# Kernel tuning notes

Hardware: AMD Instinct MI355X
Metric: run time of the kernel (lower is better)

The kernel has to match this reference:

```python
import jax, jax.numpy as jnp
import numpy as np

B, L, C, H = 1, 2048, 2048, 16
D = C // H
EPS = 1e-6
W0 = 30.0  # SIREN frequency

def rmsnorm(x, w, eps=EPS):
    return x * jax.lax.rsqrt(jnp.mean(x * x, axis=-1, keepdims=True) + eps) * w

def depth_rope(x, depth, base=10000.0):
    # same rotation for all positions, angle set by scalar layer depth
    d = x.shape[-1]
    half = d // 2
    freqs = 1.0 / base ** (jnp.arange(half, dtype=x.dtype) / half)
    ang = depth * freqs
    cos, sin = jnp.cos(ang), jnp.sin(ang)
    x1, x2 = x[..., :half], x[..., half:2 * half]
    return jnp.concatenate([x1 * cos - x2 * sin, x1 * sin + x2 * cos], axis=-1)

def setup_inputs() -> dict:
    key = jax.random.key(0)
    ks = jax.random.split(key, 13)
    s = 1.0 / np.sqrt(C)
    inp = {
        'x':  jax.random.normal(ks[0], (B, L, C), jnp.float32),
        'h0': jax.random.normal(ks[1], (B, L, C), jnp.float32),
        'h1': jax.random.normal(ks[2], (B, L, C), jnp.float32),
        'h2': jax.random.normal(ks[3], (B, L, C), jnp.float32),
        'Wq': jax.random.normal(ks[4], (C, C), jnp.float32) * s,
        'Wk': jax.random.normal(ks[5], (C, C), jnp.float32) * s,
        'Wv': jax.random.normal(ks[6], (C, C), jnp.float32) * s,
        'Wo': jax.random.normal(ks[7], (C, C), jnp.float32) * s,
        'qn_w': jnp.ones((D,), jnp.float32),
        'kn_w': jnp.ones((D,), jnp.float32),
        'on_w': jnp.ones((C,), jnp.float32),
        'sw1': jax.random.normal(ks[8], (1, C), jnp.float32),
        'sb1': jax.random.normal(ks[9], (C,), jnp.float32) * 0.01,
        'sw2': jax.random.normal(ks[10], (C, C), jnp.float32) * s,
        'sb2': jnp.zeros((C,), jnp.float32),
    }
    return inp

def reference(x, h0, h1, h2, Wq, Wk, Wv, Wo, qn_w, kn_w, on_w, sw1, sb1, sw2, sb2):
    history = [h0, h1, h2]
    q_src = history[-1]                      # [B,L,C]
    q_depth = len(history) - 1
    # Q path: proj -> per-head RMSNorm -> depth RoPE
    q = jnp.einsum('blc,oc->blo', q_src, Wq).reshape(B, L, H, D)
    q = depth_rope(rmsnorm(q, qn_w), q_depth)
    # K/V path over prior history entries (each with its own depth)
    k_parts, v_parts = [], []
    for depth_idx, kv in enumerate(history[:-1]):
        k_i = jnp.einsum('blc,oc->blo', kv, Wk).reshape(B, L, H, D)
        v_i = jnp.einsum('blc,oc->blo', kv, Wv).reshape(B, L, H, D)
        k_parts.append(depth_rope(rmsnorm(k_i, kn_w), depth_idx))
        v_parts.append(v_i)
    k = jnp.concatenate(k_parts, axis=1)     # [B,Lkv,H,D]
    v = jnp.concatenate(v_parts, axis=1)
    # full SDPA, default scale D^-0.5
    scores = jnp.einsum('bqhd,bkhd->bhqk', q, k) * (D ** -0.5)
    attn = jax.nn.softmax(scores, axis=-1)
    out = jnp.einsum('bhqk,bkhd->bqhd', attn, v).reshape(B, L, C)
    out = jnp.einsum('blc,oc->blo', out, Wo)
    # SIREN upsample to (L,): target length == L -> identity interpolation
    # plus sine-activated coordinate MLP (implicit positional field)
    coords = jnp.linspace(-1.0, 1.0, L, dtype=x.dtype)[:, None]   # [L,1]
    pos = jnp.sin(W0 * (coords @ sw1 + sb1)) @ sw2 + sb2           # [L,C]
    out = out + pos[None]
    return x + rmsnorm(out, on_w)
```

## Files before the change

### kernel.cpp

```cpp
#include <hip/hip_runtime.h>
#include <hip/hip_fp16.h>

#define LQ 2048
#define CDIM 2048
#define NHEAD 16
#define HDIM 128
#define LKEY 4096

typedef _Float16 f16x8 __attribute__((ext_vector_type(8)));
typedef float f32x4 __attribute__((ext_vector_type(4)));

#define GLOAD_LDS16(g, s) __builtin_amdgcn_global_load_lds( \
    (const __attribute__((address_space(1))) void*)(g),     \
    (__attribute__((address_space(3))) void*)(s), 16, 0, 0)

#define MFMA16(a, b, c) __builtin_amdgcn_mfma_f32_16x16x32_f16(a, b, c, 0, 0, 0)

__device__ __forceinline__ void storeC(float* p, float v) { *p = v; }
__device__ __forceinline__ void storeC(__half* p, float v) { *p = __float2half(v); }
__device__ __forceinline__ float toF(float v) { return v; }
__device__ __forceinline__ float toF(__half v) { return __half2float(v); }

template <typename OutT>
__global__ __launch_bounds__(256, 2) void gemm_bt(
    const __half* __restrict__ A, const __half* __restrict__ B,
    OutT* __restrict__ C, int lda, int ldb, int ldc, int K)
{
    __shared__ __align__(16) __half lA[128 * 64];
    __shared__ __align__(16) __half lB[128 * 64];
    const int tid  = threadIdx.x;
    const int lane = tid & 63;
    const int wave = tid >> 6;
    const int bm = blockIdx.x, bn = blockIdx.y;
    const int r = tid >> 3;
    const int g = tid & 7;
    const __half* gA = A + (long)(bm * 128 + r) * lda + ((g ^ (r & 7)) << 3);
    const __half* gB = B + (long)(bn * 128 + r) * ldb + ((g ^ (r & 7)) << 3);
    __half* lAp = lA + tid * 8;
    __half* lBp = lB + tid * 8;
    const int wr = (wave & 1) << 6;
    const int wc = (wave >> 1) << 6;
    const int l15 = lane & 15, quad = lane >> 4;

    f32x4 acc[4][4] = {};

    for (int kt = 0; kt < K; kt += 64) {
#pragma unroll
        for (int i = 0; i < 4; ++i) {
            GLOAD_LDS16(gA + (long)i * 32 * lda, lAp + i * 2048);
            GLOAD_LDS16(gB + (long)i * 32 * ldb, lBp + i * 2048);
        }
        gA += 64; gB += 64;
        __syncthreads();
#pragma unroll
        for (int kk = 0; kk < 2; ++kk) {
            f16x8 af[4], bfr[4];
#pragma unroll
            for (int mi = 0; mi < 4; ++mi) {
                const int m = wr + mi * 16 + l15;
                const int kg = kk * 4 + quad;
                af[mi] = *(const f16x8*)&lA[m * 64 + ((kg ^ (m & 7)) << 3)];
            }
#pragma unroll
            for (int ni = 0; ni < 4; ++ni) {
                const int n = wc + ni * 16 + l15;
                const int kg = kk * 4 + quad;
                bfr[ni] = *(const f16x8*)&lB[n * 64 + ((kg ^ (n & 7)) << 3)];
            }
#pragma unroll
            for (int mi = 0; mi < 4; ++mi)
#pragma unroll
                for (int ni = 0; ni < 4; ++ni)
                    acc[mi][ni] = MFMA16(af[mi], bfr[ni], acc[mi][ni]);
        }
        __syncthreads();
    }
    const int row0 = bm * 128 + wr + quad * 4;
    const int col0 = bn * 128 + wc + l15;
#pragma unroll
    for (int mi = 0; mi < 4; ++mi)
#pragma unroll
        for (int ni = 0; ni < 4; ++ni)
#pragma unroll
            for (int rx = 0; rx < 4; ++rx)
                storeC(&C[(long)(row0 + mi * 16 + rx) * ldc + col0 + ni * 16],
                       acc[mi][ni][rx]);
}

__global__ __launch_bounds__(256, 2) void attn_tile(
    const __half* __restrict__ Qf,
    const __half* __restrict__ Kf,
    const __half* __restrict__ Vt,
    float* __restrict__ Opart,
    float* __restrict__ lsum)
{
    __shared__ __align__(16) __half lK[64 * 128];
    __shared__ __align__(16) __half lV[128 * 64];
    __shared__ __align__(16) __half pL[4 * 2 * 16 * 72];

    const int tid  = threadIdx.x;
    const int lane = tid & 63;
    const int wave = tid >> 6;
    const int l15  = lane & 15;
    const int quad = lane >> 4;
    const int h  = blockIdx.y >> 1;
    const int kc = blockIdx.y & 1;
    const int q0 = blockIdx.x * 128 + wave * 32;

    f16x8 aq[2][4];
#pragma unroll
    for (int mt = 0; mt < 2; ++mt)
#pragma unroll
        for (int ks = 0; ks < 4; ++ks)
            aq[mt][ks] = *(const f16x8*)&Qf[(long)(q0 + mt * 16 + l15) * CDIM +
                                            h * HDIM + ks * 32 + quad * 8];

    const int rK = tid >> 4;
    const int gK = tid & 15;
    const __half* srcK = Kf + (long)(kc * 2048 + rK) * 4096 + h * HDIM +
                         ((gK ^ (rK & 15)) << 3);
    const int rV = tid >> 3;
    const int gV = tid & 7;
    const __half* srcV = Vt + (long)(h * HDIM + rV) * (long)LKEY + kc * 2048 +
                         ((gV ^ (rV & 7)) << 3);
    __half* dstK = lK + tid * 8;
    __half* dstV = lV + tid * 8;

    f32x4 accO[2][8] = {};
    f32x4 l_acc[2] = {};

    for (int st = 0; st < 32; ++st) {
#pragma unroll
        for (int i = 0; i < 4; ++i) {
            GLOAD_LDS16(srcK + (long)(st * 64 + i * 16) * 4096, dstK + i * 2048);
            GLOAD_LDS16(srcV + (long)i * 32 * LKEY + st * 64, dstV + i * 2048);
        }
        __syncthreads();
        f32x4 s[2][4];
#pragma unroll
        for (int mt = 0; mt < 2; ++mt)
#pragma unroll
            for (int nt = 0; nt < 4; ++nt)
                s[mt][nt] = (f32x4){-10.f, -10.f, -10.f, -10.f};
#pragma unroll
        for (int nt = 0; nt < 4; ++nt) {
            const int n = nt * 16 + l15;
#pragma unroll
            for (int ks = 0; ks < 4; ++ks) {
                const f16x8 kf = *(const f16x8*)
                    &lK[n * 128 + (((ks * 4 + quad) ^ (n & 15)) << 3)];
                s[0][nt] = MFMA16(aq[0][ks], kf, s[0][nt]);
                s[1][nt] = MFMA16(aq[1][ks], kf, s[1][nt]);
            }
        }
#pragma unroll
        for (int mt = 0; mt < 2; ++mt)
#pragma unroll
            for (int nt = 0; nt < 4; ++nt)
#pragma unroll
                for (int r2 = 0; r2 < 4; ++r2) {
                    const float p = __builtin_amdgcn_exp2f(s[mt][nt][r2]);
                    l_acc[mt][r2] += p;
                    pL[((wave * 2 + mt) * 16 + quad * 4 + r2) * 72 +
                       nt * 16 + l15] = __float2half(p);
                }
        f16x8 ap[2][2];
#pragma unroll
        for (int mt = 0; mt < 2; ++mt) {
            ap[mt][0] = *(const f16x8*)&pL[((wave * 2 + mt) * 16 + l15) * 72 + quad * 8];
            ap[mt][1] = *(const f16x8*)&pL[((wave * 2 + mt) * 16 + l15) * 72 + 32 + quad * 8];
        }
#pragma unroll
        for (int nt2 = 0; nt2 < 8; ++nt2) {
            const int n2 = nt2 * 16 + l15;
            const f16x8 v0 = *(const f16x8*)&lV[n2 * 64 + ((quad ^ (n2 & 7)) << 3)];
            const f16x8 v1 = *(const f16x8*)&lV[n2 * 64 + (((4 + quad) ^ (n2 & 7)) << 3)];
            accO[0][nt2] = MFMA16(ap[0][0], v0, accO[0][nt2]);
            accO[0][nt2] = MFMA16(ap[0][1], v1, accO[0][nt2]);
            accO[1][nt2] = MFMA16(ap[1][0], v0, accO[1][nt2]);
            accO[1][nt2] = MFMA16(ap[1][1], v1, accO[1][nt2]);
        }
        __syncthreads();
    }

#pragma unroll
    for (int mt = 0; mt < 2; ++mt)
#pragma unroll
        for (int r2 = 0; r2 < 4; ++r2) {
            float v = l_acc[mt][r2];
            v += __shfl_xor(v, 1);
            v += __shfl_xor(v, 2);
            v += __shfl_xor(v, 4);
            v += __shfl_xor(v, 8);
            if (l15 == 0)
                atomicAdd(&lsum[h * LQ + q0 + mt * 16 + quad * 4 + r2], v);
        }
    float* Cp = Opart + (long)kc * LQ * CDIM + h * HDIM;
#pragma unroll
    for (int mt = 0; mt < 2; ++mt)
#pragma unroll
        for (int nt2 = 0; nt2 < 8; ++nt2)
#pragma unroll
            for (int rx = 0; rx < 4; ++rx)
                Cp[(long)(q0 + mt * 16 + quad * 4 + rx) * CDIM + nt2 * 16 + l15] =
                    accO[mt][nt2][rx];
}

__global__ __launch_bounds__(256) void merge_o(
    const float* __restrict__ Op, const float* __restrict__ lsum,
    __half* __restrict__ a2)
{
    const int row = blockIdx.x;
    const int c0  = threadIdx.x * 8;
    const float inv = 1.0f / lsum[(c0 >> 7) * LQ + row];
    const float* p0 = Op + (long)row * CDIM + c0;
    const float* p1 = p0 + (long)LQ * CDIM;
    union { f16x8 v; _Float16 e[8]; } o;
#pragma unroll
    for (int j = 0; j < 8; ++j)
        o.e[j] = (_Float16)((p0[j] + p1[j]) * inv);
    *(f16x8*)&a2[(long)row * 4096 + c0] = o.v;
}

__global__ __launch_bounds__(256) void norm_rope(
    __half* __restrict__ X, const float* __restrict__ w,
    int stride, int nrows, int kmode, float oscale)
{
    const int gid  = blockIdx.x * 4 + (threadIdx.x >> 6);
    const int lane = threadIdx.x & 63;
    const int row  = gid >> 4;
    const int h    = gid & 15;
    if (row >= nrows) return;
    __half* p = X + (long)row * stride + h * HDIM;
    float x1 = __half2float(p[lane]);
    float x2 = __half2float(p[lane + 64]);
    float ss = x1 * x1 + x2 * x2;
#pragma unroll
    for (int off = 1; off < 64; off <<= 1) ss += __shfl_xor(ss, off);
    const float rn = rsqrtf(ss * (1.0f / 128.0f) + 1e-6f);
    x1 *= rn * w[lane];
    x2 *= rn * w[lane + 64];
    const int depth = kmode ? (row < LQ ? 0 : 1) : 2;
    const float freq = exp2f(-(float)lane * 0.20762050593045702f);
    const float ang = (float)depth * freq;
    float sn, cs;
    __sincosf(ang, &sn, &cs);
    p[lane]      = __float2half((x1 * cs - x2 * sn) * oscale);
    p[lane + 64] = __float2half((x1 * sn + x2 * cs) * oscale);
}

__global__ void cast_h4(const float* __restrict__ in, __half* __restrict__ out, int n) {
    const int i = (blockIdx.x * 256 + threadIdx.x) << 2;
    if (i >= n) return;
    const float4 v = *(const float4*)&in[i];
    out[i]     = __float2half(v.x);
    out[i + 1] = __float2half(v.y);
    out[i + 2] = __float2half(v.z);
    out[i + 3] = __float2half(v.w);
}

__global__ void cast_wo(const float* __restrict__ in, __half* __restrict__ out) {
    const int idx = blockIdx.x * 256 + threadIdx.x;
    const int o = idx >> 11, c = idx & 2047;
    out[((long)o << 12) + c] = __float2half(in[idx]);
}

template <typename InT>
__global__ __launch_bounds__(256) void transpose_h(
    const InT* __restrict__ in, long inStride, long inOff,
    __half* __restrict__ out, long outStride, long outOff)
{
    __shared__ float t[64][65];
    const long r0 = (long)blockIdx.x * 64;
    const long c0 = (long)blockIdx.y * 64;
    const int tj = threadIdx.x & 63;
    const int ti = threadIdx.x >> 6;
#pragma unroll
    for (int it = 0; it < 16; ++it) {
        const int i = it * 4 + ti;
        t[i][tj] = toF(in[(r0 + i) * inStride + inOff + c0 + tj]);
    }
    __syncthreads();
#pragma unroll
    for (int it = 0; it < 16; ++it) {
        const int i = it * 4 + ti;
        out[(c0 + i) * outStride + outOff + r0 + tj] = __float2half(t[tj][i]);
    }
}

__global__ void sin_feat(const float* __restrict__ sw1, const float* __restrict__ sb1,
                         __half* __restrict__ a2) {
    const int idx = blockIdx.x * 256 + threadIdx.x;
    const int l = idx >> 11, c = idx & 2047;
    const float coord = -1.0f + (2.0f / 2047.0f) * (float)l;
    const float v = sinf(30.0f * (coord * sw1[c] + sb1[c]));
    a2[((long)l << 12) + 2048 + c] = __float2half(v);
}

__global__ __launch_bounds__(256) void final_norm(
    const float* __restrict__ out2, const float* __restrict__ x,
    const float* __restrict__ sb2, const float* __restrict__ on_w,
    float* __restrict__ y)
{
    const int row = blockIdx.x;
    const float* o = out2 + (long)row * CDIM;
    float v[8];
    float ss = 0.f;
#pragma unroll
    for (int i = 0; i < 8; ++i) {
        const int c = threadIdx.x + i * 256;
        const float t = o[c] + sb2[c];
        v[i] = t;
        ss += t * t;
    }
#pragma unroll
    for (int off = 1; off < 64; off <<= 1) ss += __shfl_xor(ss, off);
    __shared__ float red[4];
    const int lane = threadIdx.x & 63, wv = threadIdx.x >> 6;
    if (lane == 0) red[wv] = ss;
    __syncthreads();
    const float tot = red[0] + red[1] + red[2] + red[3];
    const float rn = rsqrtf(tot * (1.0f / 2048.0f) + 1e-6f);
#pragma unroll
    for (int i = 0; i < 8; ++i) {
        const int c = threadIdx.x + i * 256;
        y[(long)row * CDIM + c] = x[(long)row * CDIM + c] + v[i] * rn * on_w[c];
    }
}

extern "C" void kernel_launch(void* const* d_in, const int* in_sizes, int n_in,
                              void* d_out, int out_size, void* d_ws, size_t ws_size,
                              hipStream_t stream) {
    const float* x    = (const float*)d_in[0];
    const float* h0   = (const float*)d_in[1];
    const float* h1   = (const float*)d_in[2];
    const float* h2   = (const float*)d_in[3];
    const float* Wq   = (const float*)d_in[4];
    const float* Wk   = (const float*)d_in[5];
    const float* Wv   = (const float*)d_in[6];
    const float* Wo   = (const float*)d_in[7];
    const float* qn_w = (const float*)d_in[8];
    const float* kn_w = (const float*)d_in[9];
    const float* on_w = (const float*)d_in[10];
    const float* sw1  = (const float*)d_in[11];
    const float* sb1  = (const float*)d_in[12];
    const float* sw2  = (const float*)d_in[13];
    const float* sb2  = (const float*)d_in[14];
    float* y = (float*)d_out;

    const size_t MB = 1ull << 20;
    char* w = (char*)d_ws;
    __half* xq  = (__half*)(w);
    __half* xkv = (__half*)(w + 8 * MB);
    __half* wqh = (__half*)(w + 24 * MB);
    __half* wkv = (__half*)(w + 32 * MB);
    __half* qf  = (__half*)(w + 48 * MB);
    __half* kvf = (__half*)(w + 56 * MB);
    __half* vT  = (__half*)(w + 88 * MB);
    __half* a2  = (__half*)(w + 104 * MB);
    __half* b2  = (__half*)(w + 120 * MB);
    float* out2 = (float*)(w + 136 * MB);
    float* Opart = (float*)(w);
    float* lsum  = (float*)(w + 32 * MB);
    (void)in_sizes; (void)n_in; (void)out_size; (void)ws_size;

    const int n4 = 2048 * 2048;
    cast_h4<<<n4 / 1024, 256, 0, stream>>>(h2, xq, n4);
    cast_h4<<<n4 / 1024, 256, 0, stream>>>(h0, xkv, n4);
    cast_h4<<<n4 / 1024, 256, 0, stream>>>(h1, xkv + n4, n4);
    cast_h4<<<n4 / 1024, 256, 0, stream>>>(Wq, wqh, n4);
    cast_h4<<<n4 / 1024, 256, 0, stream>>>(Wk, wkv, n4);
    cast_h4<<<n4 / 1024, 256, 0, stream>>>(Wv, wkv + n4, n4);
    cast_wo<<<n4 / 256, 256, 0, stream>>>(Wo, b2);
    transpose_h<float><<<dim3(32, 32), 256, 0, stream>>>(sw2, 2048, 0, b2, 4096, 2048);
    sin_feat<<<n4 / 256, 256, 0, stream>>>(sw1, sb1, a2);

    gemm_bt<__half><<<dim3(16, 16), 256, 0, stream>>>(xq, wqh, qf, 2048, 2048, 2048, 2048);
    gemm_bt<__half><<<dim3(32, 32), 256, 0, stream>>>(xkv, wkv, kvf, 2048, 2048, 4096, 2048);

    norm_rope<<<8192, 256, 0, stream>>>(qf, qn_w, 2048, 2048, 0, 0.12751743f);
    norm_rope<<<16384, 256, 0, stream>>>(kvf, kn_w, 4096, 4096, 1, 1.0f);
    transpose_h<__half><<<dim3(64, 32), 256, 0, stream>>>(kvf, 4096, 2048, vT, 4096, 0);

    (void)hipMemsetAsync(lsum, 0, NHEAD * LQ * sizeof(float), stream);
    attn_tile<<<dim3(16, 32), 256, 0, stream>>>(qf, kvf, vT, Opart, lsum);
    merge_o<<<2048, 256, 0, stream>>>(Opart, lsum, a2);

    gemm_bt<float><<<dim3(16, 16), 256, 0, stream>>>(a2, b2, out2, 4096, 4096, 2048, 4096);
    final_norm<<<2048, 256, 0, stream>>>(out2, x, sb2, on_w, y);
}
```

Before: 525.9 us.

## Merge QKV GEMMs, split-K output GEMM, fuse casts, vectorize sin features

Combines the Q and KV projection GEMMs into one launch, addressing the KV input through its fixed offset after the Q input. The final GEMM is split along K into two partial outputs, which the final norm kernel sums, to expose more blocks than the 256-block launch. The six cast kernels are fused into one with vectorized half stores, and sin_feat is vectorized using fast __sinf. The attention P buffer row pitch is padded to reduce LDS bank conflicts. Risks are the added partial-sum traffic and lower accuracy from __sinf with large arguments.

```diff
diff --git a/kernel.cpp b/kernel.cpp
--- a/kernel.cpp
+++ b/kernel.cpp
@@ -8,6 +8,7 @@
 #define LKEY 4096
 
 typedef _Float16 f16x8 __attribute__((ext_vector_type(8)));
+typedef _Float16 f16x4 __attribute__((ext_vector_type(4)));
 typedef float f32x4 __attribute__((ext_vector_type(4)));
 
 #define GLOAD_LDS16(g, s) __builtin_amdgcn_global_load_lds( \
@@ -22,19 +23,19 @@
 __device__ __forceinline__ float toF(__half v) { return __half2float(v); }
 
 template <typename OutT>
-__global__ __launch_bounds__(256, 2) void gemm_bt(
+__device__ __forceinline__ void gemm_body(
     const __half* __restrict__ A, const __half* __restrict__ B,
-    OutT* __restrict__ C, int lda, int ldb, int ldc, int K)
+    OutT* __restrict__ C, int lda, int ldb, int ldc, int K,
+    int bmA, int bmC, int bn)
 {
     __shared__ __align__(16) __half lA[128 * 64];
     __shared__ __align__(16) __half lB[128 * 64];
     const int tid  = threadIdx.x;
     const int lane = tid & 63;
     const int wave = tid >> 6;
-    const int bm = blockIdx.x, bn = blockIdx.y;
     const int r = tid >> 3;
     const int g = tid & 7;
-    const __half* gA = A + (long)(bm * 128 + r) * lda + ((g ^ (r & 7)) << 3);
+    const __half* gA = A + (long)(bmA * 128 + r) * lda + ((g ^ (r & 7)) << 3);
     const __half* gB = B + (long)(bn * 128 + r) * ldb + ((g ^ (r & 7)) << 3);
     __half* lAp = lA + tid * 8;
     __half* lBp = lB + tid * 8;
@@ -75,7 +76,7 @@
         }
         __syncthreads();
     }
-    const int row0 = bm * 128 + wr + quad * 4;
+    const int row0 = bmC * 128 + wr + quad * 4;
     const int col0 = bn * 128 + wc + l15;
 #pragma unroll
     for (int mi = 0; mi < 4; ++mi)
@@ -85,6 +86,31 @@
             for (int rx = 0; rx < 4; ++rx)
                 storeC(&C[(long)(row0 + mi * 16 + rx) * ldc + col0 + ni * 16],
                        acc[mi][ni][rx]);
+}
+
+__global__ __launch_bounds__(256, 2) void gemm_qkv(
+    const __half* __restrict__ A, const __half* __restrict__ Bq,
+    const __half* __restrict__ Bkv, __half* __restrict__ Cq,
+    __half* __restrict__ Ckv)
+{
+    const int lin = blockIdx.x;
+    if (lin < 1024) {
+        const int bm = lin & 31, bn = lin >> 5;
+        gemm_body<__half>(A, Bkv, Ckv, 2048, 2048, 4096, 2048, bm + 16, bm, bn);
+    } else {
+        const int l2 = lin - 1024;
+        const int bm = l2 & 15, bn = l2 >> 4;
+        gemm_body<__half>(A, Bq, Cq, 2048, 2048, 2048, 2048, bm, bm, bn);
+    }
+}
+
+__global__ __launch_bounds__(256, 2) void gemm_sk(
+    const __half* __restrict__ A, const __half* __restrict__ B,
+    float* __restrict__ C, int lda, int ldb, int ldc, int Khalf)
+{
+    const int z = blockIdx.z;
+    gemm_body<float>(A + z * Khalf, B + z * Khalf, C + (long)z * LQ * CDIM,
+                     lda, ldb, ldc, Khalf, blockIdx.x, blockIdx.x, blockIdx.y);
 }
 
 __global__ __launch_bounds__(256, 2) void attn_tile(
@@ -96,7 +122,7 @@
 {
     __shared__ __align__(16) __half lK[64 * 128];
     __shared__ __align__(16) __half lV[128 * 64];
-    __shared__ __align__(16) __half pL[4 * 2 * 16 * 72];
+    __shared__ __align__(16) __half pL[4 * 2 * 16 * 76];
 
     const int tid  = threadIdx.x;
     const int lane = tid & 63;
@@ -161,14 +187,14 @@
                 for (int r2 = 0; r2 < 4; ++r2) {
                     const float p = __builtin_amdgcn_exp2f(s[mt][nt][r2]);
                     l_acc[mt][r2] += p;
-                    pL[((wave * 2 + mt) * 16 + quad * 4 + r2) * 72 +
+                    pL[((wave * 2 + mt) * 16 + quad * 4 + r2) * 76 +
                        nt * 16 + l15] = __float2half(p);
                 }
         f16x8 ap[2][2];
 #pragma unroll
         for (int mt = 0; mt < 2; ++mt) {
-            ap[mt][0] = *(const f16x8*)&pL[((wave * 2 + mt) * 16 + l15) * 72 + quad * 8];
-            ap[mt][1] = *(const f16x8*)&pL[((wave * 2 + mt) * 16 + l15) * 72 + 32 + quad * 8];
+            ap[mt][0] = *(const f16x8*)&pL[((wave * 2 + mt) * 16 + l15) * 76 + quad * 8];
+            ap[mt][1] = *(const f16x8*)&pL[((wave * 2 + mt) * 16 + l15) * 76 + 32 + quad * 8];
         }
 #pragma unroll
         for (int nt2 = 0; nt2 < 8; ++nt2) {
@@ -249,14 +275,30 @@
     p[lane + 64] = __float2half((x1 * sn + x2 * cs) * oscale);
 }
 
-__global__ void cast_h4(const float* __restrict__ in, __half* __restrict__ out, int n) {
-    const int i = (blockIdx.x * 256 + threadIdx.x) << 2;
-    if (i >= n) return;
-    const float4 v = *(const float4*)&in[i];
-    out[i]     = __float2half(v.x);
-    out[i + 1] = __float2half(v.y);
-    out[i + 2] = __float2half(v.z);
-    out[i + 3] = __float2half(v.w);
+__global__ __launch_bounds__(256) void cast_all(
+    const float* __restrict__ h2, const float* __restrict__ h0,
+    const float* __restrict__ h1, const float* __restrict__ Wq,
+    const float* __restrict__ Wk, const float* __restrict__ Wv,
+    __half* __restrict__ xq, __half* __restrict__ xkv,
+    __half* __restrict__ wqh, __half* __restrict__ wkv)
+{
+    const long i = ((long)blockIdx.x * 256 + threadIdx.x) << 2;
+    const int chunk = (int)(i >> 22);
+    const long off = i & 4194303;
+    const float* s; __half* d;
+    switch (chunk) {
+        case 0:  s = h2; d = xq;            break;
+        case 1:  s = h0; d = xkv;           break;
+        case 2:  s = h1; d = xkv + 4194304; break;
+        case 3:  s = Wq; d = wqh;           break;
+        case 4:  s = Wk; d = wkv;           break;
+        default: s = Wv; d = wkv + 4194304; break;
+    }
+    const float4 v = *(const float4*)&s[off];
+    f16x4 o;
+    o[0] = (_Float16)v.x; o[1] = (_Float16)v.y;
+    o[2] = (_Float16)v.z; o[3] = (_Float16)v.w;
+    *(f16x4*)&d[off] = o;
 }
 
 __global__ void cast_wo(const float* __restrict__ in, __half* __restrict__ out) {
@@ -288,13 +330,21 @@
     }
 }
 
-__global__ void sin_feat(const float* __restrict__ sw1, const float* __restrict__ sb1,
-                         __half* __restrict__ a2) {
-    const int idx = blockIdx.x * 256 + threadIdx.x;
+__global__ __launch_bounds__(256) void sin_feat(
+    const float* __restrict__ sw1, const float* __restrict__ sb1,
+    __half* __restrict__ a2)
+{
+    const int idx = (blockIdx.x * 256 + threadIdx.x) << 2;
     const int l = idx >> 11, c = idx & 2047;
     const float coord = -1.0f + (2.0f / 2047.0f) * (float)l;
-    const float v = sinf(30.0f * (coord * sw1[c] + sb1[c]));
-    a2[((long)l << 12) + 2048 + c] = __float2half(v);
+    const float4 w = *(const float4*)&sw1[c];
+    const float4 b = *(const float4*)&sb1[c];
+    f16x4 o;
+    o[0] = (_Float16)__sinf(30.0f * (coord * w.x + b.x));
+    o[1] = (_Float16)__sinf(30.0f * (coord * w.y + b.y));
+    o[2] = (_Float16)__sinf(30.0f * (coord * w.z + b.z));
+    o[3] = (_Float16)__sinf(30.0f * (coord * w.w + b.w));
+    *(f16x4*)&a2[((long)l << 12) + 2048 + c] = o;
 }
 
 __global__ __launch_bounds__(256) void final_norm(
@@ -303,13 +353,14 @@
     float* __restrict__ y)
 {
     const int row = blockIdx.x;
-    const float* o = out2 + (long)row * CDIM;
+    const float* o0 = out2 + (long)row * CDIM;
+    const float* o1 = o0 + (long)LQ * CDIM;
     float v[8];
     float ss = 0.f;
 #pragma unroll
     for (int i = 0; i < 8; ++i) {
         const int c = threadIdx.x + i * 256;
-        const float t = o[c] + sb2[c];
+        const float t = o0[c] + o1[c] + sb2[c];
         v[i] = t;
         ss += t * t;
     }
@@ -359,24 +410,18 @@
     __half* vT  = (__half*)(w + 88 * MB);
     __half* a2  = (__half*)(w + 104 * MB);
     __half* b2  = (__half*)(w + 120 * MB);
-    float* out2 = (float*)(w + 136 * MB);
     float* Opart = (float*)(w);
     float* lsum  = (float*)(w + 32 * MB);
+    float* out2  = (float*)(w + 56 * MB);
     (void)in_sizes; (void)n_in; (void)out_size; (void)ws_size;
 
     const int n4 = 2048 * 2048;
-    cast_h4<<<n4 / 1024, 256, 0, stream>>>(h2, xq, n4);
-    cast_h4<<<n4 / 1024, 256, 0, stream>>>(h0, xkv, n4);
-    cast_h4<<<n4 / 1024, 256, 0, stream>>>(h1, xkv + n4, n4);
-    cast_h4<<<n4 / 1024, 256, 0, stream>>>(Wq, wqh, n4);
-    cast_h4<<<n4 / 1024, 256, 0, stream>>>(Wk, wkv, n4);
-    cast_h4<<<n4 / 1024, 256, 0, stream>>>(Wv, wkv + n4, n4);
+    cast_all<<<24576, 256, 0, stream>>>(h2, h0, h1, Wq, Wk, Wv, xq, xkv, wqh, wkv);
     cast_wo<<<n4 / 256, 256, 0, stream>>>(Wo, b2);
     transpose_h<float><<<dim3(32, 32), 256, 0, stream>>>(sw2, 2048, 0, b2, 4096, 2048);
-    sin_feat<<<n4 / 256, 256, 0, stream>>>(sw1, sb1, a2);
-
-    gemm_bt<__half><<<dim3(16, 16), 256, 0, stream>>>(xq, wqh, qf, 2048, 2048, 2048, 2048);
-    gemm_bt<__half><<<dim3(32, 32), 256, 0, stream>>>(xkv, wkv, kvf, 2048, 2048, 4096, 2048);
+    sin_feat<<<4096, 256, 0, stream>>>(sw1, sb1, a2);
+
+    gemm_qkv<<<1280, 256, 0, stream>>>(xq, wqh, wkv, qf, kvf);
 
     norm_rope<<<8192, 256, 0, stream>>>(qf, qn_w, 2048, 2048, 0, 0.12751743f);
     norm_rope<<<16384, 256, 0, stream>>>(kvf, kn_w, 4096, 4096, 1, 1.0f);
@@ -386,6 +431,6 @@
     attn_tile<<<dim3(16, 32), 256, 0, stream>>>(qf, kvf, vT, Opart, lsum);
     merge_o<<<2048, 256, 0, stream>>>(Opart, lsum, a2);
 
-    gemm_bt<float><<<dim3(16, 16), 256, 0, stream>>>(a2, b2, out2, 4096, 4096, 2048, 4096);
+    gemm_sk<<<dim3(16, 16, 2), 256, 0, stream>>>(a2, b2, out2, 4096, 4096, 2048, 2048);
     final_norm<<<2048, 256, 0, stream>>>(out2, x, sb2, on_w, y);
 }
```

Measured after the change: 454.1 us. 1.16x faster.
